# Optimization experiments

Measured on AMD Instinct MI355X. Metric: run time of the kernel, lower is better.

## Reference

```python
import jax, jax.numpy as jnp
import numpy as np

NS, NW, E, DIN, OUT, H = 100_000, 400_000, 500_000, 64, 64, 4


def setup_inputs() -> dict:
    key = jax.random.key(0)
    ks = jax.random.split(key, 26)
    s = 1.0 / np.sqrt(DIN)
    sg = 1.0 / np.sqrt(OUT)
    inp = {
        "x_sites": jax.random.normal(ks[0], (NS, DIN), jnp.float32),
        "x_wells": jax.random.normal(ks[1], (NW, DIN), jnp.float32),
        "edge_sw_src": jax.random.randint(ks[2], (E,), 0, NS, jnp.int32),
        "edge_sw_dst": jax.random.randint(ks[3], (E,), 0, NW, jnp.int32),
        "edge_ws_src": jax.random.randint(ks[4], (E,), 0, NW, jnp.int32),
        "edge_ws_dst": jax.random.randint(ks[5], (E,), 0, NS, jnp.int32),
        # GAT ('pfas_sites','distance','gw_wells'), heads=4, concat=False
        "W_sw": jax.random.normal(ks[6], (DIN, H * OUT), jnp.float32) * s,
        "att_src_sw": jax.random.normal(ks[7], (H, OUT), jnp.float32) * sg,
        "att_dst_sw": jax.random.normal(ks[8], (H, OUT), jnp.float32) * sg,
        "b_sw": jnp.zeros((OUT,), jnp.float32),
        # SAGE ('gw_wells','distance','pfas_sites')
        "Wl_ws": jax.random.normal(ks[9], (DIN, OUT), jnp.float32) * s,
        "bl_ws": jnp.zeros((OUT,), jnp.float32),
        "Wr_ws": jax.random.normal(ks[10], (DIN, OUT), jnp.float32) * s,
        # GAT ('pfas_sites','self_loop','pfas_sites'), add_self_loops=True -> identity edges
        "W_ss": jax.random.normal(ks[11], (DIN, H * OUT), jnp.float32) * s,
        "att_src_ss": jax.random.normal(ks[12], (H, OUT), jnp.float32) * sg,
        "att_dst_ss": jax.random.normal(ks[13], (H, OUT), jnp.float32) * sg,
        "b_ss": jnp.zeros((OUT,), jnp.float32),
        # SAGE ('gw_wells','self_loop','gw_wells') with identity edges
        "Wl_ww": jax.random.normal(ks[14], (DIN, OUT), jnp.float32) * s,
        "bl_ww": jnp.zeros((OUT,), jnp.float32),
        "Wr_ww": jax.random.normal(ks[15], (DIN, OUT), jnp.float32) * s,
        # output heads
        "Wg": jax.random.normal(ks[16], (OUT, 1), jnp.float32) * sg,
        "bg": jnp.zeros((1,), jnp.float32),
        "Wsit": jax.random.normal(ks[17], (OUT, 1), jnp.float32) * sg,
        "bsit": jnp.zeros((1,), jnp.float32),
    }
    return inp


def _gat(x_src, x_dst, src, dst, W, a_src, a_dst, b, n_dst):
    """PyG GATConv, concat=False (mean over heads), negative_slope=0.2."""
    h, c = a_src.shape
    xs = (x_src @ W).reshape(-1, h, c)  # [Ns,H,C]
    xd = (x_dst @ W).reshape(-1, h, c)  # [Nd,H,C]
    al_s = jnp.einsum("nhc,hc->nh", xs, a_src)
    al_d = jnp.einsum("nhc,hc->nh", xd, a_dst)
    e = jax.nn.leaky_relu(al_s[src] + al_d[dst], 0.2)  # [E,H]
    m = jax.ops.segment_max(e, dst, num_segments=n_dst)
    ex = jnp.exp(e - m[dst])
    denom = jax.ops.segment_sum(ex, dst, num_segments=n_dst)
    alpha = ex / denom[dst]  # edge-softmax per dst node
    msg = xs[src] * alpha[:, :, None]  # [E,H,C] dominant intermediate
    out = jax.ops.segment_sum(msg, dst, num_segments=n_dst)
    return out.mean(axis=1) + b


def _sage(x_src, x_dst, src, dst, Wl, bl, Wr, n_dst):
    """PyG SAGEConv, mean aggregation, root_weight=True."""
    ssum = jax.ops.segment_sum(x_src[src], dst, num_segments=n_dst)
    cnt = jax.ops.segment_sum(jnp.ones((src.shape[0],), x_src.dtype), dst, num_segments=n_dst)
    mean = ssum / jnp.maximum(cnt, 1.0)[:, None]  # empty neighborhood -> 0 (PyG mean scatter)
    return mean @ Wl + bl + x_dst @ Wr


def reference(x_sites, x_wells, edge_sw_src, edge_sw_dst, edge_ws_src, edge_ws_dst,
              W_sw, att_src_sw, att_dst_sw, b_sw, Wl_ws, bl_ws, Wr_ws,
              W_ss, att_src_ss, att_dst_ss, b_ss, Wl_ww, bl_ww, Wr_ww,
              Wg, bg, Wsit, bsit):
    # relation 1: GAT sites -> wells
    gw = _gat(x_sites, x_wells, edge_sw_src, edge_sw_dst, W_sw, att_src_sw, att_dst_sw, b_sw, NW)
    # relation 4: SAGE self-loop on wells; identity edges -> mean == x itself
    gw = gw + (x_wells @ Wl_ww + bl_ww + x_wells @ Wr_ww)  # HeteroConv aggr='sum'
    # relation 2: SAGE wells -> sites
    si = _sage(x_wells, x_sites, edge_ws_src, edge_ws_dst, Wl_ws, bl_ws, Wr_ws, NS)
    # relation 3: GAT self-loop on sites (add_self_loops=True -> identity edge set);
    # softmax over a single self edge is 1, so output = mean over heads of lin(x) + bias
    si = si + (x_sites @ W_ss).reshape(NS, H, OUT).mean(axis=1) + b_ss
    # post: relu -> dropout (eval mode: identity) -> linear -> leaky_relu(0.01)
    gw = jax.nn.relu(gw)
    si = jax.nn.relu(si)
    o_gw = jax.nn.leaky_relu(gw @ Wg + bg, 0.01)   # [NW, 1]
    o_si = jax.nn.leaky_relu(si @ Wsit + bsit, 0.01)  # [NS, 1]
    return o_gw, o_si
```

## Files before the change

### kernel.cpp

```cpp
#include <hip/hip_runtime.h>

#define NS_ 100000
#define NW_ 400000
#define NE_ 500000
#define EPB 2048

typedef float f32x4_t __attribute__((ext_vector_type(4)));
typedef unsigned u32x4_t __attribute__((ext_vector_type(4)));

__device__ __forceinline__ float lrelu02(float x) { return x > 0.f ? x : 0.2f * x; }
__device__ __forceinline__ float bf2f(unsigned short u) {
    return __uint_as_float(((unsigned)u) << 16);
}
__device__ __forceinline__ unsigned short f2bf(float f) {
    unsigned u = __float_as_uint(f);
    u += 0x7FFFu + ((u >> 16) & 1u);
    return (unsigned short)(u >> 16);
}
__device__ __forceinline__ unsigned pk(float lo, float hi) {
    return (unsigned)f2bf(lo) | ((unsigned)f2bf(hi) << 16);
}
__device__ __forceinline__ void mfma_bf16(f32x4_t& acc, u32x4_t a, u32x4_t b) {
    asm volatile("v_mfma_f32_16x16x32_bf16 %0, %1, %2, %0" : "+v"(acc) : "v"(a), "v"(b));
}

__global__ void __launch_bounds__(256)
k_prep(const float* __restrict__ W_sw, const float* __restrict__ att_src,
       const float* __restrict__ att_dst,
       const float* __restrict__ Wl_ww, const float* __restrict__ Wr_ww,
       const float* __restrict__ Wl_ws, const float* __restrict__ Wr_ws,
       const float* __restrict__ W_ss,
       float* __restrict__ vd, float* __restrict__ vs,
       u32x4_t* __restrict__ fw, u32x4_t* __restrict__ fs,
       u32x4_t* __restrict__ fsp)
{
    const int tid = threadIdx.x;
    {
        int d = tid >> 2, h = tid & 3;
        const float4* wp = (const float4*)(W_sw + d * 256 + h * 64);
        const float4* ad = (const float4*)(att_dst + h * 64);
        const float4* as = (const float4*)(att_src + h * 64);
        float accd = 0.f, accs = 0.f;
#pragma unroll
        for (int c = 0; c < 16; ++c) {
            float4 wv = wp[c]; float4 dv = ad[c]; float4 sv = as[c];
            accd += wv.x * dv.x + wv.y * dv.y + wv.z * dv.z + wv.w * dv.w;
            accs += wv.x * sv.x + wv.y * sv.y + wv.z * sv.z + wv.w * sv.w;
        }
        vd[d * 4 + h] = accd;
        vs[d * 4 + h] = accs;
    }
    for (int idx = tid; idx < 512; idx += 256) {
        int f = idx >> 6, lane = idx & 63;
        int kc = f >> 2, ct = f & 3, q = lane >> 4, n = lane & 15;
        int c = ct * 16 + n;
        u32x4_t d;
#pragma unroll
        for (int i = 0; i < 4; ++i) {
            int k = kc * 32 + q * 8 + 2 * i;
            d[i] = pk(Wl_ww[k * 64 + c] + Wr_ww[k * 64 + c],
                      Wl_ww[(k + 1) * 64 + c] + Wr_ww[(k + 1) * 64 + c]);
        }
        fw[idx] = d;
    }
    for (int idx = tid; idx < 1024; idx += 256) {
        int f = idx >> 6, lane = idx & 63;
        int kc = f >> 2, ct = f & 3, q = lane >> 4, n = lane & 15;
        int c = ct * 16 + n;
        u32x4_t d;
#pragma unroll
        for (int i = 0; i < 4; ++i) {
            int k = kc * 32 + q * 8 + 2 * i;
            float lo, hi;
            if (k < 64) {
                lo = Wl_ws[k * 64 + c];
                hi = Wl_ws[(k + 1) * 64 + c];
            } else {
                int kk = k - 64;
                lo = Wr_ws[kk * 64 + c] + 0.25f * (W_ss[kk * 256 + c] + W_ss[kk * 256 + 64 + c] +
                                                   W_ss[kk * 256 + 128 + c] + W_ss[kk * 256 + 192 + c]);
                hi = Wr_ws[(kk + 1) * 64 + c] + 0.25f * (W_ss[(kk + 1) * 256 + c] + W_ss[(kk + 1) * 256 + 64 + c] +
                                                         W_ss[(kk + 1) * 256 + 128 + c] + W_ss[(kk + 1) * 256 + 192 + c]);
            }
            d[i] = pk(lo, hi);
        }
        fs[idx] = d;
    }
    for (int idx = tid; idx < 2048; idx += 256) {
        int f = idx >> 6, lane = idx & 63;
        int kc = f >> 4, ct = f & 15, q = lane >> 4, n = lane & 15;
        int c = ct * 16 + n;
        u32x4_t d;
#pragma unroll
        for (int i = 0; i < 4; ++i) {
            int k = kc * 32 + q * 8 + 2 * i;
            d[i] = pk(W_sw[k * 256 + c], W_sw[(k + 1) * 256 + c]);
        }
        fsp[idx] = d;
    }
}

#define SP_PAD 264
__global__ void __launch_bounds__(256)
k_sites_pre(const float* __restrict__ x_sites, const u32x4_t* __restrict__ fsp,
            const float* __restrict__ vs, unsigned short* __restrict__ xs,
            float* __restrict__ al_s)
{
    __shared__ unsigned short stg[4][16 * SP_PAD];
    __shared__ float vsl[256];
    const int tid = threadIdx.x;
    vsl[tid] = vs[tid];
    __syncthreads();
    const int wave = __builtin_amdgcn_readfirstlane(tid >> 6);
    const int lane = tid & 63, q = lane >> 4, n = lane & 15;
    const int sbase = blockIdx.x * 64 + wave * 16;
    const int srow = min(sbase + n, NS_ - 1);
    const float* xr = x_sites + (size_t)srow * 64 + q * 8;
    float4 x0 = *(const float4*)(xr);
    float4 x1 = *(const float4*)(xr + 4);
    float4 x2 = *(const float4*)(xr + 32);
    float4 x3 = *(const float4*)(xr + 36);
    u32x4_t am0 = { pk(x0.x, x0.y), pk(x0.z, x0.w), pk(x1.x, x1.y), pk(x1.z, x1.w) };
    u32x4_t am1 = { pk(x2.x, x2.y), pk(x2.z, x2.w), pk(x3.x, x3.y), pk(x3.z, x3.w) };
    float pa[4];
#pragma unroll
    for (int h = 0; h < 4; ++h) {
        const float* v0 = &vsl[(q * 8) * 4 + h];
        const float* v1 = &vsl[(32 + q * 8) * 4 + h];
        pa[h] = x0.x * v0[0]  + x0.y * v0[4]  + x0.z * v0[8]  + x0.w * v0[12]
              + x1.x * v0[16] + x1.y * v0[20] + x1.z * v0[24] + x1.w * v0[28]
              + x2.x * v1[0]  + x2.y * v1[4]  + x2.z * v1[8]  + x2.w * v1[12]
              + x3.x * v1[16] + x3.y * v1[20] + x3.z * v1[24] + x3.w * v1[28];
    }
#pragma unroll
    for (int h = 0; h < 4; ++h) {
        pa[h] += __shfl_xor(pa[h], 16, 64);
        pa[h] += __shfl_xor(pa[h], 32, 64);
    }
    if (q == 0 && sbase + n < NS_)
        *(float4*)(al_s + (size_t)(sbase + n) * 4) = make_float4(pa[0], pa[1], pa[2], pa[3]);

    f32x4_t acc[16];
#pragma unroll
    for (int ct = 0; ct < 16; ++ct) acc[ct] = (f32x4_t){0, 0, 0, 0};
    asm volatile("s_nop 3" : "+v"(am0), "+v"(am1));
#pragma unroll
    for (int ct = 0; ct < 16; ++ct) mfma_bf16(acc[ct], am0, fsp[ct * 64 + lane]);
#pragma unroll
    for (int ct = 0; ct < 16; ++ct) mfma_bf16(acc[ct], am1, fsp[(16 + ct) * 64 + lane]);
    asm volatile("s_nop 7\n\ts_nop 7" ::: "memory");
    unsigned short* ss = &stg[wave][0];
#pragma unroll
    for (int ct = 0; ct < 16; ++ct)
#pragma unroll
        for (int reg = 0; reg < 4; ++reg)
            ss[(q * 4 + reg) * SP_PAD + ct * 16 + n] = f2bf(acc[ct][reg]);
    __builtin_amdgcn_s_waitcnt(0);
#pragma unroll
    for (int i = 0; i < 8; ++i) {
        int g = i * 64 + lane;
        int r = g >> 5, c = g & 31;
        if (sbase + r < NS_) {
            u32x4_t v = *(const u32x4_t*)(ss + r * SP_PAD + c * 8);
            *(u32x4_t*)(xs + (size_t)(sbase + r) * 256 + c * 8) = v;
        }
    }
}

__global__ void __launch_bounds__(256)
k_hist2(const int* __restrict__ d1, int* __restrict__ h1,
        const int* __restrict__ d2, int* __restrict__ h2)
{
    int e = blockIdx.x * 256 + threadIdx.x;
    if (e >= NE_) return;
    if (blockIdx.y == 0) atomicAdd(&h1[d1[e]], 1);
    else                 atomicAdd(&h2[d2[e]], 1);
}

__global__ void __launch_bounds__(256)
k_scan1_2(const int* __restrict__ h1, int n1, int* __restrict__ b1, int nb1,
          const int* __restrict__ h2, int n2, int* __restrict__ b2)
{
    __shared__ int red[256];
    const int tid = threadIdx.x;
    const int bx = blockIdx.x;
    const int* hist; int n; int* bsum; int blk;
    if (bx < nb1) { hist = h1; n = n1; bsum = b1; blk = bx; }
    else          { hist = h2; n = n2; bsum = b2; blk = bx - nb1; }
    int base = blk * EPB + tid * 8;
    int s = 0;
#pragma unroll
    for (int i = 0; i < 8; ++i) { int idx = base + i; if (idx < n) s += hist[idx]; }
    red[tid] = s;
    __syncthreads();
    for (int off = 128; off > 0; off >>= 1) {
        if (tid < off) red[tid] += red[tid + off];
        __syncthreads();
    }
    if (tid == 0) bsum[blk] = red[0];
}

__global__ void __launch_bounds__(256)
k_scan2_2(int* __restrict__ b1, int nb1, int* __restrict__ b2, int nb2)
{
    __shared__ int sh[256];
    const int tid = threadIdx.x;
    int* bsum = blockIdx.x == 0 ? b1 : b2;
    int nb = blockIdx.x == 0 ? nb1 : nb2;
    sh[tid] = (tid < nb) ? bsum[tid] : 0;
    __syncthreads();
    for (int off = 1; off < 256; off <<= 1) {
        int u = (tid >= off) ? sh[tid - off] : 0;
        __syncthreads();
        sh[tid] += u;
        __syncthreads();
    }
    if (tid < nb) bsum[tid] = (tid == 0) ? 0 : sh[tid - 1];
}

__global__ void __launch_bounds__(256)
k_scan3_2(const int* __restrict__ h1, int n1, const int* __restrict__ b1,
          int* __restrict__ rp1, int* __restrict__ cu1, int nb1,
          const int* __restrict__ h2, int n2, const int* __restrict__ b2,
          int* __restrict__ rp2, int* __restrict__ cu2)
{
    __shared__ int tsum[256];
    const int tid = threadIdx.x;
    const int bx = blockIdx.x;
    const int* hist; int n; const int* bsum; int* rowptr; int* cursor; int blk;
    if (bx < nb1) { hist = h1; n = n1; bsum = b1; rowptr = rp1; cursor = cu1; blk = bx; }
    else          { hist = h2; n = n2; bsum = b2; rowptr = rp2; cursor = cu2; blk = bx - nb1; }
    int base = blk * EPB + tid * 8;
    int v[8]; int s = 0;
#pragma unroll
    for (int i = 0; i < 8; ++i) {
        int idx = base + i;
        v[i] = (idx < n) ? hist[idx] : 0;
        s += v[i];
    }
    tsum[tid] = s;
    __syncthreads();
    for (int off = 1; off < 256; off <<= 1) {
        int u = (tid >= off) ? tsum[tid - off] : 0;
        __syncthreads();
        tsum[tid] += u;
        __syncthreads();
    }
    int texcl = tsum[tid] - s;
    int run = bsum[blk] + texcl;
#pragma unroll
    for (int i = 0; i < 8; ++i) {
        int idx = base + i;
        if (idx < n) { rowptr[idx] = run; cursor[idx] = run; run += v[i]; }
    }
    if (blk == 0 && tid == 0) rowptr[n] = NE_;
}

__global__ void __launch_bounds__(256)
k_scatter2(const int* __restrict__ s1, const int* __restrict__ d1,
           int* __restrict__ c1, int* __restrict__ o1,
           const int* __restrict__ s2, const int* __restrict__ d2,
           int* __restrict__ c2, int* __restrict__ o2)
{
    int e = blockIdx.x * 256 + threadIdx.x;
    if (e >= NE_) return;
    if (blockIdx.y == 0) { int p = atomicAdd(&c1[d1[e]], 1); o1[p] = s1[e]; }
    else                 { int p = atomicAdd(&c2[d2[e]], 1); o2[p] = s2[e]; }
}

__global__ void __launch_bounds__(256)
k_gat_wells(const float* __restrict__ x_wells, const float* __restrict__ vd,
            const int* __restrict__ rowptr, const int* __restrict__ csr_src,
            const float* __restrict__ al_s, const unsigned short* __restrict__ xs,
            const float* __restrict__ b_sw, const float* __restrict__ bl_ww,
            const u32x4_t* __restrict__ fw, const float* __restrict__ Wg,
            const float* __restrict__ bg, float* __restrict__ out)
{
    __shared__ float vdl[16][17];
    __shared__ float xw[16][68];
    __shared__ float dl[16][68];
    __shared__ float biasl[64];
    __shared__ float wgl[64];
    __shared__ float res[16];
    const int tid = threadIdx.x;
    vdl[tid >> 4][tid & 15] = vd[tid];
    if (tid < 64) { biasl[tid] = b_sw[tid] + bl_ww[tid]; wgl[tid] = Wg[tid]; }
    __syncthreads();
    const int wl = tid >> 4, p = tid & 15;
    const int w = blockIdx.x * 16 + wl;
    float h0, h1, h2, h3;
    {
        float4 xv = *(const float4*)(x_wells + (size_t)w * 64 + 4 * p);
        *(float4*)&xw[wl][4 * p] = xv;
        const float* vp = vdl[p];
        h0 = xv.x * vp[0] + xv.y * vp[4] + xv.z * vp[8]  + xv.w * vp[12];
        h1 = xv.x * vp[1] + xv.y * vp[5] + xv.z * vp[9]  + xv.w * vp[13];
        h2 = xv.x * vp[2] + xv.y * vp[6] + xv.z * vp[10] + xv.w * vp[14];
        h3 = xv.x * vp[3] + xv.y * vp[7] + xv.z * vp[11] + xv.w * vp[15];
    }
#pragma unroll
    for (int off = 1; off < 16; off <<= 1) {
        h0 += __shfl_xor(h0, off, 64);
        h1 += __shfl_xor(h1, off, 64);
        h2 += __shfl_xor(h2, off, 64);
        h3 += __shfl_xor(h3, off, 64);
    }
    const int r0 = rowptr[w], r1 = rowptr[w + 1];
    float den0 = 0, den1 = 0, den2 = 0, den3 = 0;
    float n0[4] = {0, 0, 0, 0}, n1[4] = {0, 0, 0, 0};
    float n2[4] = {0, 0, 0, 0}, n3[4] = {0, 0, 0, 0};
    for (int j = r0; j < r1; ++j) {
        int s = csr_src[j];
        float4 as = ((const float4*)al_s)[s];
        float e0 = __expf(lrelu02(as.x + h0));
        float e1 = __expf(lrelu02(as.y + h1));
        float e2 = __expf(lrelu02(as.z + h2));
        float e3 = __expf(lrelu02(as.w + h3));
        den0 += e0; den1 += e1; den2 += e2; den3 += e3;
        const unsigned short* xr = xs + (size_t)s * 256 + 4 * p;
        ushort4 u0 = *(const ushort4*)(xr);
        ushort4 u1 = *(const ushort4*)(xr + 64);
        ushort4 u2 = *(const ushort4*)(xr + 128);
        ushort4 u3 = *(const ushort4*)(xr + 192);
        n0[0] += e0 * bf2f(u0.x); n0[1] += e0 * bf2f(u0.y); n0[2] += e0 * bf2f(u0.z); n0[3] += e0 * bf2f(u0.w);
        n1[0] += e1 * bf2f(u1.x); n1[1] += e1 * bf2f(u1.y); n1[2] += e1 * bf2f(u1.z); n1[3] += e1 * bf2f(u1.w);
        n2[0] += e2 * bf2f(u2.x); n2[1] += e2 * bf2f(u2.y); n2[2] += e2 * bf2f(u2.z); n2[3] += e2 * bf2f(u2.w);
        n3[0] += e3 * bf2f(u3.x); n3[1] += e3 * bf2f(u3.y); n3[2] += e3 * bf2f(u3.z); n3[3] += e3 * bf2f(u3.w);
    }
    const int c0 = 4 * p;
    float tmsg[4];
    if (r1 > r0) {
        float i0 = 0.25f / den0, i1 = 0.25f / den1, i2 = 0.25f / den2, i3 = 0.25f / den3;
#pragma unroll
        for (int i = 0; i < 4; ++i)
            tmsg[i] = n0[i] * i0 + n1[i] * i1 + n2[i] * i2 + n3[i] * i3 + biasl[c0 + i];
    } else {
#pragma unroll
        for (int i = 0; i < 4; ++i) tmsg[i] = biasl[c0 + i];
    }
    __syncthreads();
    const int wave = __builtin_amdgcn_readfirstlane(tid >> 6);
    const int lane = tid & 63, q = lane >> 4, n = lane & 15;
    u32x4_t a0, a1;
#pragma unroll
    for (int i = 0; i < 4; ++i) {
        a0[i] = pk(xw[n][q * 8 + 2 * i],      xw[n][q * 8 + 2 * i + 1]);
        a1[i] = pk(xw[n][32 + q * 8 + 2 * i], xw[n][32 + q * 8 + 2 * i + 1]);
    }
    f32x4_t acc = {0, 0, 0, 0};
    asm volatile("s_nop 3" : "+v"(a0), "+v"(a1), "+v"(acc));
    mfma_bf16(acc, a0, fw[wave * 64 + lane]);
    mfma_bf16(acc, a1, fw[(4 + wave) * 64 + lane]);
    asm volatile("s_nop 7\n\ts_nop 7" : "+v"(acc));
#pragma unroll
    for (int reg = 0; reg < 4; ++reg)
        dl[q * 4 + reg][wave * 16 + n] = acc[reg];
    __syncthreads();
    float4 dv = *(const float4*)&dl[wl][c0];
    float t0 = tmsg[0] + dv.x;
    float t1 = tmsg[1] + dv.y;
    float t2 = tmsg[2] + dv.z;
    float t3 = tmsg[3] + dv.w;
    float pr = fmaxf(t0, 0.f) * wgl[c0] + fmaxf(t1, 0.f) * wgl[c0 + 1] +
               fmaxf(t2, 0.f) * wgl[c0 + 2] + fmaxf(t3, 0.f) * wgl[c0 + 3];
    pr += __shfl_xor(pr, 1, 64);
    pr += __shfl_xor(pr, 2, 64);
    pr += __shfl_xor(pr, 4, 64);
    pr += __shfl_xor(pr, 8, 64);
    if (p == 0) res[wl] = pr + bg[0];
    __syncthreads();
    if (tid < 16) {
        float v = res[tid];
        out[blockIdx.x * 16 + tid] = v > 0.f ? v : 0.01f * v;
    }
}

__global__ void __launch_bounds__(256)
k_sage_sites(const float* __restrict__ x_sites, const float* __restrict__ x_wells,
             const int* __restrict__ rowptr, const int* __restrict__ csr_src,
             const u32x4_t* __restrict__ fs, const float* __restrict__ bl_ws,
             const float* __restrict__ b_ss, const float* __restrict__ Wsit,
             const float* __restrict__ bsit, float* __restrict__ out)
{
    __shared__ float mnL[16][68];
    __shared__ float xL[16][68];
    __shared__ float dl[16][68];
    __shared__ float biasl[64];
    __shared__ float wsl[64];
    __shared__ float res[16];
    const int tid = threadIdx.x;
    if (tid < 64) { biasl[tid] = bl_ws[tid] + b_ss[tid]; wsl[tid] = Wsit[tid]; }
    const int sl = tid >> 4, p = tid & 15;
    const int s = blockIdx.x * 16 + sl;
    const int r0 = rowptr[s], r1 = rowptr[s + 1];
    float4 m4 = {0.f, 0.f, 0.f, 0.f};
    for (int j = r0; j < r1; ++j) {
        int wsrc = csr_src[j];
        float4 xv = ((const float4*)(x_wells + (size_t)wsrc * 64))[p];
        m4.x += xv.x; m4.y += xv.y; m4.z += xv.z; m4.w += xv.w;
    }
    if (r1 > r0) {
        float rc = 1.f / (float)(r1 - r0);
        m4.x *= rc; m4.y *= rc; m4.z *= rc; m4.w *= rc;
    }
    *(float4*)&mnL[sl][4 * p] = m4;
    {
        float4 xv = *(const float4*)(x_sites + (size_t)s * 64 + 4 * p);
        *(float4*)&xL[sl][4 * p] = xv;
    }
    __syncthreads();
    const int wave = __builtin_amdgcn_readfirstlane(tid >> 6);
    const int lane = tid & 63, q = lane >> 4, n = lane & 15;
    u32x4_t am0, am1, ax0, ax1;
#pragma unroll
    for (int i = 0; i < 4; ++i) {
        am0[i] = pk(mnL[n][q * 8 + 2 * i],      mnL[n][q * 8 + 2 * i + 1]);
        am1[i] = pk(mnL[n][32 + q * 8 + 2 * i], mnL[n][32 + q * 8 + 2 * i + 1]);
        ax0[i] = pk(xL[n][q * 8 + 2 * i],       xL[n][q * 8 + 2 * i + 1]);
        ax1[i] = pk(xL[n][32 + q * 8 + 2 * i],  xL[n][32 + q * 8 + 2 * i + 1]);
    }
    f32x4_t acc = {0, 0, 0, 0};
    asm volatile("s_nop 3" : "+v"(am0), "+v"(am1), "+v"(ax0), "+v"(ax1), "+v"(acc));
    mfma_bf16(acc, am0, fs[wave * 64 + lane]);
    mfma_bf16(acc, am1, fs[(4 + wave) * 64 + lane]);
    mfma_bf16(acc, ax0, fs[(8 + wave) * 64 + lane]);
    mfma_bf16(acc, ax1, fs[(12 + wave) * 64 + lane]);
    asm volatile("s_nop 7\n\ts_nop 7" : "+v"(acc));
#pragma unroll
    for (int reg = 0; reg < 4; ++reg)
        dl[q * 4 + reg][wave * 16 + n] = acc[reg];
    __syncthreads();
    const int c0 = 4 * p;
    float4 dv = *(const float4*)&dl[sl][c0];
    float t0 = dv.x + biasl[c0];
    float t1 = dv.y + biasl[c0 + 1];
    float t2 = dv.z + biasl[c0 + 2];
    float t3 = dv.w + biasl[c0 + 3];
    float pr = fmaxf(t0, 0.f) * wsl[c0] + fmaxf(t1, 0.f) * wsl[c0 + 1] +
               fmaxf(t2, 0.f) * wsl[c0 + 2] + fmaxf(t3, 0.f) * wsl[c0 + 3];
    pr += __shfl_xor(pr, 1, 64);
    pr += __shfl_xor(pr, 2, 64);
    pr += __shfl_xor(pr, 4, 64);
    pr += __shfl_xor(pr, 8, 64);
    if (p == 0) res[sl] = pr + bsit[0];
    __syncthreads();
    if (tid < 16) {
        float v = res[tid];
        out[(size_t)NW_ + blockIdx.x * 16 + tid] = v > 0.f ? v : 0.01f * v;
    }
}

extern "C" void kernel_launch(void* const* d_in, const int* in_sizes, int n_in,
                              void* d_out, int out_size, void* d_ws, size_t ws_size,
                              hipStream_t stream)
{
    const float* x_sites    = (const float*)d_in[0];
    const float* x_wells    = (const float*)d_in[1];
    const int*   e_sw_src   = (const int*)d_in[2];
    const int*   e_sw_dst   = (const int*)d_in[3];
    const int*   e_ws_src   = (const int*)d_in[4];
    const int*   e_ws_dst   = (const int*)d_in[5];
    const float* W_sw       = (const float*)d_in[6];
    const float* att_src_sw = (const float*)d_in[7];
    const float* att_dst_sw = (const float*)d_in[8];
    const float* b_sw       = (const float*)d_in[9];
    const float* Wl_ws      = (const float*)d_in[10];
    const float* bl_ws      = (const float*)d_in[11];
    const float* Wr_ws      = (const float*)d_in[12];
    const float* W_ss       = (const float*)d_in[13];
    const float* b_ss       = (const float*)d_in[16];
    const float* Wl_ww      = (const float*)d_in[17];
    const float* bl_ww      = (const float*)d_in[18];
    const float* Wr_ww      = (const float*)d_in[19];
    const float* Wg         = (const float*)d_in[20];
    const float* bg         = (const float*)d_in[21];
    const float* Wsit       = (const float*)d_in[22];
    const float* bsit       = (const float*)d_in[23];
    float* out = (float*)d_out;

    unsigned short* xs = (unsigned short*)d_ws;
    float* al_s = (float*)(xs + (size_t)NS_ * 256);
    float* vd   = al_s + (size_t)NS_ * 4;
    float* vs   = vd + 256;
    u32x4_t* fw = (u32x4_t*)(vs + 256);
    u32x4_t* fs = fw + 512;
    u32x4_t* fsp= fs + 1024;
    int* ip     = (int*)(fsp + 2048);
    int* h_sw   = ip;
    int* h_ws   = h_sw + NW_;
    int* rp_sw  = h_ws + NS_;
    int* cur_sw = rp_sw + NW_ + 4;
    int* csr_sw = cur_sw + NW_;
    int* bs_sw  = csr_sw + NE_;
    int* rp_ws  = bs_sw + 256;
    int* cur_ws = rp_ws + NS_ + 4;
    int* csr_ws = cur_ws + NS_;
    int* bs_ws  = csr_ws + NE_;

    hipMemsetAsync(h_sw, 0, (size_t)(NW_ + NS_) * sizeof(int), stream);

    const int egrid = (NE_ + 255) / 256;
    const int nb_sw = (NW_ + EPB - 1) / EPB;
    const int nb_ws = (NS_ + EPB - 1) / EPB;

    hipLaunchKernelGGL(k_hist2, dim3(egrid, 2), dim3(256), 0, stream,
                       e_sw_dst, h_sw, e_ws_dst, h_ws);
    hipLaunchKernelGGL(k_scan1_2, dim3(nb_sw + nb_ws), dim3(256), 0, stream,
                       h_sw, NW_, bs_sw, nb_sw, h_ws, NS_, bs_ws);
    hipLaunchKernelGGL(k_scan2_2, dim3(2), dim3(256), 0, stream,
                       bs_sw, nb_sw, bs_ws, nb_ws);
    hipLaunchKernelGGL(k_scan3_2, dim3(nb_sw + nb_ws), dim3(256), 0, stream,
                       h_sw, NW_, bs_sw, rp_sw, cur_sw, nb_sw,
                       h_ws, NS_, bs_ws, rp_ws, cur_ws);
    hipLaunchKernelGGL(k_scatter2, dim3(egrid, 2), dim3(256), 0, stream,
                       e_sw_src, e_sw_dst, cur_sw, csr_sw,
                       e_ws_src, e_ws_dst, cur_ws, csr_ws);

    hipLaunchKernelGGL(k_prep, dim3(1), dim3(256), 0, stream,
                       W_sw, att_src_sw, att_dst_sw, Wl_ww, Wr_ww, Wl_ws, Wr_ws, W_ss,
                       vd, vs, fw, fs, fsp);
    hipLaunchKernelGGL(k_sites_pre, dim3((NS_ + 63) / 64), dim3(256), 0, stream,
                       x_sites, fsp, vs, xs, al_s);

    hipLaunchKernelGGL(k_gat_wells, dim3(NW_ / 16), dim3(256), 0, stream,
                       x_wells, vd, rp_sw, csr_sw, al_s, xs, b_sw, bl_ww,
                       fw, Wg, bg, out);
    hipLaunchKernelGGL(k_sage_sites, dim3(NS_ / 16), dim3(256), 0, stream,
                       x_sites, x_wells, rp_ws, csr_ws, fs, bl_ws, b_ss,
                       Wsit, bsit, out);
}
```

Measured before the change: 468.5 us.

## Merge independent kernels into combined launches and pack bf16 tiles in LDS

Merges the sites precompute with the degree histogram into one launch, moves the weight prep before it, and fuses the SAGE-sites and GAT-wells aggregation kernels into one grid that branches on block index. The MFMA input tiles are now packed to bf16 when written to shared memory with a swizzled layout, instead of being converted from fp32 when read back. The goal is fewer kernel launches and inter-kernel gaps, tail overlap between independent work, and less shared-memory traffic. The cost is a larger shared-memory footprint per block in the merged kernels, which may lower occupancy for the lighter branch.

```diff
diff --git a/kernel.cpp b/kernel.cpp
--- a/kernel.cpp
+++ b/kernel.cpp
@@ -4,6 +4,11 @@
 #define NW_ 400000
 #define NE_ 500000
 #define EPB 2048
+
+#define SP_BLKS  ((NS_ + 63) / 64)
+#define HG_BLKS  ((NE_ + 255) / 256)
+#define SAGE_BLKS (NS_ / 16)
+#define GAT_BLKS  (NW_ / 16)
 
 typedef float f32x4_t __attribute__((ext_vector_type(4)));
 typedef unsigned u32x4_t __attribute__((ext_vector_type(4)));
@@ -102,18 +107,33 @@
 
 #define SP_PAD 264
 __global__ void __launch_bounds__(256)
-k_sites_pre(const float* __restrict__ x_sites, const u32x4_t* __restrict__ fsp,
-            const float* __restrict__ vs, unsigned short* __restrict__ xs,
-            float* __restrict__ al_s)
-{
-    __shared__ unsigned short stg[4][16 * SP_PAD];
-    __shared__ float vsl[256];
+k_main1(const float* __restrict__ x_sites, const u32x4_t* __restrict__ fsp,
+        const float* __restrict__ vs, unsigned short* __restrict__ xs,
+        float* __restrict__ al_s,
+        const int* __restrict__ d1, int* __restrict__ h1,
+        const int* __restrict__ d2, int* __restrict__ h2)
+{
+    __shared__ float smem1[8704];
     const int tid = threadIdx.x;
+    const int bid = blockIdx.x;
+    if (bid >= SP_BLKS) {
+        int hb = bid - SP_BLKS;
+        int rel = hb / HG_BLKS;
+        int e = (hb % HG_BLKS) * 256 + tid;
+        if (e < NE_) {
+            if (rel == 0) atomicAdd(&h1[d1[e]], 1);
+            else          atomicAdd(&h2[d2[e]], 1);
+        }
+        return;
+    }
+    unsigned short* stg = (unsigned short*)smem1;
+    float* vsl = smem1 + 8448 / 2 * 0 + 8448;
+    vsl = smem1 + 8448;
     vsl[tid] = vs[tid];
     __syncthreads();
     const int wave = __builtin_amdgcn_readfirstlane(tid >> 6);
     const int lane = tid & 63, q = lane >> 4, n = lane & 15;
-    const int sbase = blockIdx.x * 64 + wave * 16;
+    const int sbase = bid * 64 + wave * 16;
     const int srow = min(sbase + n, NS_ - 1);
     const float* xr = x_sites + (size_t)srow * 64 + q * 8;
     float4 x0 = *(const float4*)(xr);
@@ -149,7 +169,7 @@
 #pragma unroll
     for (int ct = 0; ct < 16; ++ct) mfma_bf16(acc[ct], am1, fsp[(16 + ct) * 64 + lane]);
     asm volatile("s_nop 7\n\ts_nop 7" ::: "memory");
-    unsigned short* ss = &stg[wave][0];
+    unsigned short* ss = stg + wave * (16 * SP_PAD);
 #pragma unroll
     for (int ct = 0; ct < 16; ++ct)
 #pragma unroll
@@ -165,16 +185,6 @@
             *(u32x4_t*)(xs + (size_t)(sbase + r) * 256 + c * 8) = v;
         }
     }
-}
-
-__global__ void __launch_bounds__(256)
-k_hist2(const int* __restrict__ d1, int* __restrict__ h1,
-        const int* __restrict__ d2, int* __restrict__ h2)
-{
-    int e = blockIdx.x * 256 + threadIdx.x;
-    if (e >= NE_) return;
-    if (blockIdx.y == 0) atomicAdd(&h1[d1[e]], 1);
-    else                 atomicAdd(&h2[d2[e]], 1);
 }
 
 __global__ void __launch_bounds__(256)
@@ -269,184 +279,190 @@
 }
 
 __global__ void __launch_bounds__(256)
-k_gat_wells(const float* __restrict__ x_wells, const float* __restrict__ vd,
-            const int* __restrict__ rowptr, const int* __restrict__ csr_src,
-            const float* __restrict__ al_s, const unsigned short* __restrict__ xs,
-            const float* __restrict__ b_sw, const float* __restrict__ bl_ww,
-            const u32x4_t* __restrict__ fw, const float* __restrict__ Wg,
-            const float* __restrict__ bg, float* __restrict__ out)
-{
-    __shared__ float vdl[16][17];
-    __shared__ float xw[16][68];
-    __shared__ float dl[16][68];
-    __shared__ float biasl[64];
-    __shared__ float wgl[64];
-    __shared__ float res[16];
+k_main6(const float* __restrict__ x_sites, const float* __restrict__ x_wells,
+        const int* __restrict__ rp_ws, const int* __restrict__ csr_ws,
+        const u32x4_t* __restrict__ fs, const float* __restrict__ bl_ws,
+        const float* __restrict__ b_ss, const float* __restrict__ Wsit,
+        const float* __restrict__ bsit,
+        const float* __restrict__ vd, const int* __restrict__ rp_sw,
+        const int* __restrict__ csr_sw, const float* __restrict__ al_s,
+        const unsigned short* __restrict__ xs, const float* __restrict__ b_sw,
+        const float* __restrict__ bl_ww, const u32x4_t* __restrict__ fw,
+        const float* __restrict__ Wg, const float* __restrict__ bg,
+        float* __restrict__ out)
+{
+    __shared__ float smem[2400];
     const int tid = threadIdx.x;
-    vdl[tid >> 4][tid & 15] = vd[tid];
-    if (tid < 64) { biasl[tid] = b_sw[tid] + bl_ww[tid]; wgl[tid] = Wg[tid]; }
-    __syncthreads();
-    const int wl = tid >> 4, p = tid & 15;
-    const int w = blockIdx.x * 16 + wl;
-    float h0, h1, h2, h3;
+    const int bid = blockIdx.x;
+
+    if (bid < SAGE_BLKS) {
+        unsigned* mnB = (unsigned*)smem;
+        unsigned* xB  = (unsigned*)(smem + 576);
+        float* dl     = smem + 1152;
+        float* biasl  = smem + 2240;
+        float* wsl    = smem + 2304;
+        float* res    = smem + 2368;
+        if (tid < 64) { biasl[tid] = bl_ws[tid] + b_ss[tid]; wsl[tid] = Wsit[tid]; }
+        const int sl = tid >> 4, p = tid & 15;
+        const int s = bid * 16 + sl;
+        const int r0 = rp_ws[s], r1 = rp_ws[s + 1];
+        float4 m4 = {0.f, 0.f, 0.f, 0.f};
+        for (int j = r0; j < r1; ++j) {
+            int wsrc = csr_ws[j];
+            float4 xv = ((const float4*)(x_wells + (size_t)wsrc * 64))[p];
+            m4.x += xv.x; m4.y += xv.y; m4.z += xv.z; m4.w += xv.w;
+        }
+        if (r1 > r0) {
+            float rc = 1.f / (float)(r1 - r0);
+            m4.x *= rc; m4.y *= rc; m4.z *= rc; m4.w *= rc;
+        }
+        {
+            int c0 = (2 * p + 8 * sl) & 31;
+            mnB[sl * 36 + c0]     = pk(m4.x, m4.y);
+            mnB[sl * 36 + c0 + 1] = pk(m4.z, m4.w);
+            float4 xv = *(const float4*)(x_sites + (size_t)s * 64 + 4 * p);
+            xB[sl * 36 + c0]     = pk(xv.x, xv.y);
+            xB[sl * 36 + c0 + 1] = pk(xv.z, xv.w);
+        }
+        __syncthreads();
+        const int wave = __builtin_amdgcn_readfirstlane(tid >> 6);
+        const int lane = tid & 63, q = lane >> 4, n = lane & 15;
+        const int b0 = (4 * q + 8 * n) & 31;
+        const int b1 = (16 + 4 * q + 8 * n) & 31;
+        u32x4_t am0 = *(const u32x4_t*)&mnB[n * 36 + b0];
+        u32x4_t am1 = *(const u32x4_t*)&mnB[n * 36 + b1];
+        u32x4_t ax0 = *(const u32x4_t*)&xB[n * 36 + b0];
+        u32x4_t ax1 = *(const u32x4_t*)&xB[n * 36 + b1];
+        f32x4_t acc = {0, 0, 0, 0};
+        asm volatile("s_nop 3" : "+v"(am0), "+v"(am1), "+v"(ax0), "+v"(ax1), "+v"(acc));
+        mfma_bf16(acc, am0, fs[wave * 64 + lane]);
+        mfma_bf16(acc, am1, fs[(4 + wave) * 64 + lane]);
+        mfma_bf16(acc, ax0, fs[(8 + wave) * 64 + lane]);
+        mfma_bf16(acc, ax1, fs[(12 + wave) * 64 + lane]);
+        asm volatile("s_nop 7\n\ts_nop 7" : "+v"(acc));
+#pragma unroll
+        for (int reg = 0; reg < 4; ++reg)
+            dl[(q * 4 + reg) * 68 + wave * 16 + n] = acc[reg];
+        __syncthreads();
+        const int c0 = 4 * p;
+        float4 dv = *(const float4*)&dl[sl * 68 + c0];
+        float t0 = dv.x + biasl[c0];
+        float t1 = dv.y + biasl[c0 + 1];
+        float t2 = dv.z + biasl[c0 + 2];
+        float t3 = dv.w + biasl[c0 + 3];
+        float pr = fmaxf(t0, 0.f) * wsl[c0] + fmaxf(t1, 0.f) * wsl[c0 + 1] +
+                   fmaxf(t2, 0.f) * wsl[c0 + 2] + fmaxf(t3, 0.f) * wsl[c0 + 3];
+        pr += __shfl_xor(pr, 1, 64);
+        pr += __shfl_xor(pr, 2, 64);
+        pr += __shfl_xor(pr, 4, 64);
+        pr += __shfl_xor(pr, 8, 64);
+        if (p == 0) res[sl] = pr + bsit[0];
+        __syncthreads();
+        if (tid < 16) {
+            float v = res[tid];
+            out[(size_t)NW_ + bid * 16 + tid] = v > 0.f ? v : 0.01f * v;
+        }
+        return;
+    }
+
     {
-        float4 xv = *(const float4*)(x_wells + (size_t)w * 64 + 4 * p);
-        *(float4*)&xw[wl][4 * p] = xv;
-        const float* vp = vdl[p];
-        h0 = xv.x * vp[0] + xv.y * vp[4] + xv.z * vp[8]  + xv.w * vp[12];
-        h1 = xv.x * vp[1] + xv.y * vp[5] + xv.z * vp[9]  + xv.w * vp[13];
-        h2 = xv.x * vp[2] + xv.y * vp[6] + xv.z * vp[10] + xv.w * vp[14];
-        h3 = xv.x * vp[3] + xv.y * vp[7] + xv.z * vp[11] + xv.w * vp[15];
-    }
-#pragma unroll
-    for (int off = 1; off < 16; off <<= 1) {
-        h0 += __shfl_xor(h0, off, 64);
-        h1 += __shfl_xor(h1, off, 64);
-        h2 += __shfl_xor(h2, off, 64);
-        h3 += __shfl_xor(h3, off, 64);
-    }
-    const int r0 = rowptr[w], r1 = rowptr[w + 1];
-    float den0 = 0, den1 = 0, den2 = 0, den3 = 0;
-    float n0[4] = {0, 0, 0, 0}, n1[4] = {0, 0, 0, 0};
-    float n2[4] = {0, 0, 0, 0}, n3[4] = {0, 0, 0, 0};
-    for (int j = r0; j < r1; ++j) {
-        int s = csr_src[j];
-        float4 as = ((const float4*)al_s)[s];
-        float e0 = __expf(lrelu02(as.x + h0));
-        float e1 = __expf(lrelu02(as.y + h1));
-        float e2 = __expf(lrelu02(as.z + h2));
-        float e3 = __expf(lrelu02(as.w + h3));
-        den0 += e0; den1 += e1; den2 += e2; den3 += e3;
-        const unsigned short* xr = xs + (size_t)s * 256 + 4 * p;
-        ushort4 u0 = *(const ushort4*)(xr);
-        ushort4 u1 = *(const ushort4*)(xr + 64);
-        ushort4 u2 = *(const ushort4*)(xr + 128);
-        ushort4 u3 = *(const ushort4*)(xr + 192);
-        n0[0] += e0 * bf2f(u0.x); n0[1] += e0 * bf2f(u0.y); n0[2] += e0 * bf2f(u0.z); n0[3] += e0 * bf2f(u0.w);
-        n1[0] += e1 * bf2f(u1.x); n1[1] += e1 * bf2f(u1.y); n1[2] += e1 * bf2f(u1.z); n1[3] += e1 * bf2f(u1.w);
-        n2[0] += e2 * bf2f(u2.x); n2[1] += e2 * bf2f(u2.y); n2[2] += e2 * bf2f(u2.z); n2[3] += e2 * bf2f(u2.w);
-        n3[0] += e3 * bf2f(u3.x); n3[1] += e3 * bf2f(u3.y); n3[2] += e3 * bf2f(u3.z); n3[3] += e3 * bf2f(u3.w);
-    }
-    const int c0 = 4 * p;
-    float tmsg[4];
-    if (r1 > r0) {
-        float i0 = 0.25f / den0, i1 = 0.25f / den1, i2 = 0.25f / den2, i3 = 0.25f / den3;
-#pragma unroll
-        for (int i = 0; i < 4; ++i)
-            tmsg[i] = n0[i] * i0 + n1[i] * i1 + n2[i] * i2 + n3[i] * i3 + biasl[c0 + i];
-    } else {
-#pragma unroll
-        for (int i = 0; i < 4; ++i) tmsg[i] = biasl[c0 + i];
-    }
-    __syncthreads();
-    const int wave = __builtin_amdgcn_readfirstlane(tid >> 6);
-    const int lane = tid & 63, q = lane >> 4, n = lane & 15;
-    u32x4_t a0, a1;
-#pragma unroll
-    for (int i = 0; i < 4; ++i) {
-        a0[i] = pk(xw[n][q * 8 + 2 * i],      xw[n][q * 8 + 2 * i + 1]);
-        a1[i] = pk(xw[n][32 + q * 8 + 2 * i], xw[n][32 + q * 8 + 2 * i + 1]);
-    }
-    f32x4_t acc = {0, 0, 0, 0};
-    asm volatile("s_nop 3" : "+v"(a0), "+v"(a1), "+v"(acc));
-    mfma_bf16(acc, a0, fw[wave * 64 + lane]);
-    mfma_bf16(acc, a1, fw[(4 + wave) * 64 + lane]);
-    asm volatile("s_nop 7\n\ts_nop 7" : "+v"(acc));
-#pragma unroll
-    for (int reg = 0; reg < 4; ++reg)
-        dl[q * 4 + reg][wave * 16 + n] = acc[reg];
-    __syncthreads();
-    float4 dv = *(const float4*)&dl[wl][c0];
-    float t0 = tmsg[0] + dv.x;
-    float t1 = tmsg[1] + dv.y;
-    float t2 = tmsg[2] + dv.z;
-    float t3 = tmsg[3] + dv.w;
-    float pr = fmaxf(t0, 0.f) * wgl[c0] + fmaxf(t1, 0.f) * wgl[c0 + 1] +
-               fmaxf(t2, 0.f) * wgl[c0 + 2] + fmaxf(t3, 0.f) * wgl[c0 + 3];
-    pr += __shfl_xor(pr, 1, 64);
-    pr += __shfl_xor(pr, 2, 64);
-    pr += __shfl_xor(pr, 4, 64);
-    pr += __shfl_xor(pr, 8, 64);
-    if (p == 0) res[wl] = pr + bg[0];
-    __syncthreads();
-    if (tid < 16) {
-        float v = res[tid];
-        out[blockIdx.x * 16 + tid] = v > 0.f ? v : 0.01f * v;
-    }
-}
-
-__global__ void __launch_bounds__(256)
-k_sage_sites(const float* __restrict__ x_sites, const float* __restrict__ x_wells,
-             const int* __restrict__ rowptr, const int* __restrict__ csr_src,
-             const u32x4_t* __restrict__ fs, const float* __restrict__ bl_ws,
-             const float* __restrict__ b_ss, const float* __restrict__ Wsit,
-             const float* __restrict__ bsit, float* __restrict__ out)
-{
-    __shared__ float mnL[16][68];
-    __shared__ float xL[16][68];
-    __shared__ float dl[16][68];
-    __shared__ float biasl[64];
-    __shared__ float wsl[64];
-    __shared__ float res[16];
-    const int tid = threadIdx.x;
-    if (tid < 64) { biasl[tid] = bl_ws[tid] + b_ss[tid]; wsl[tid] = Wsit[tid]; }
-    const int sl = tid >> 4, p = tid & 15;
-    const int s = blockIdx.x * 16 + sl;
-    const int r0 = rowptr[s], r1 = rowptr[s + 1];
-    float4 m4 = {0.f, 0.f, 0.f, 0.f};
-    for (int j = r0; j < r1; ++j) {
-        int wsrc = csr_src[j];
-        float4 xv = ((const float4*)(x_wells + (size_t)wsrc * 64))[p];
-        m4.x += xv.x; m4.y += xv.y; m4.z += xv.z; m4.w += xv.w;
-    }
-    if (r1 > r0) {
-        float rc = 1.f / (float)(r1 - r0);
-        m4.x *= rc; m4.y *= rc; m4.z *= rc; m4.w *= rc;
-    }
-    *(float4*)&mnL[sl][4 * p] = m4;
-    {
-        float4 xv = *(const float4*)(x_sites + (size_t)s * 64 + 4 * p);
-        *(float4*)&xL[sl][4 * p] = xv;
-    }
-    __syncthreads();
-    const int wave = __builtin_amdgcn_readfirstlane(tid >> 6);
-    const int lane = tid & 63, q = lane >> 4, n = lane & 15;
-    u32x4_t am0, am1, ax0, ax1;
-#pragma unroll
-    for (int i = 0; i < 4; ++i) {
-        am0[i] = pk(mnL[n][q * 8 + 2 * i],      mnL[n][q * 8 + 2 * i + 1]);
-        am1[i] = pk(mnL[n][32 + q * 8 + 2 * i], mnL[n][32 + q * 8 + 2 * i + 1]);
-        ax0[i] = pk(xL[n][q * 8 + 2 * i],       xL[n][q * 8 + 2 * i + 1]);
-        ax1[i] = pk(xL[n][32 + q * 8 + 2 * i],  xL[n][32 + q * 8 + 2 * i + 1]);
-    }
-    f32x4_t acc = {0, 0, 0, 0};
-    asm volatile("s_nop 3" : "+v"(am0), "+v"(am1), "+v"(ax0), "+v"(ax1), "+v"(acc));
-    mfma_bf16(acc, am0, fs[wave * 64 + lane]);
-    mfma_bf16(acc, am1, fs[(4 + wave) * 64 + lane]);
-    mfma_bf16(acc, ax0, fs[(8 + wave) * 64 + lane]);
-    mfma_bf16(acc, ax1, fs[(12 + wave) * 64 + lane]);
-    asm volatile("s_nop 7\n\ts_nop 7" : "+v"(acc));
-#pragma unroll
-    for (int reg = 0; reg < 4; ++reg)
-        dl[q * 4 + reg][wave * 16 + n] = acc[reg];
-    __syncthreads();
-    const int c0 = 4 * p;
-    float4 dv = *(const float4*)&dl[sl][c0];
-    float t0 = dv.x + biasl[c0];
-    float t1 = dv.y + biasl[c0 + 1];
-    float t2 = dv.z + biasl[c0 + 2];
-    float t3 = dv.w + biasl[c0 + 3];
-    float pr = fmaxf(t0, 0.f) * wsl[c0] + fmaxf(t1, 0.f) * wsl[c0 + 1] +
-               fmaxf(t2, 0.f) * wsl[c0 + 2] + fmaxf(t3, 0.f) * wsl[c0 + 3];
-    pr += __shfl_xor(pr, 1, 64);
-    pr += __shfl_xor(pr, 2, 64);
-    pr += __shfl_xor(pr, 4, 64);
-    pr += __shfl_xor(pr, 8, 64);
-    if (p == 0) res[sl] = pr + bsit[0];
-    __syncthreads();
-    if (tid < 16) {
-        float v = res[tid];
-        out[(size_t)NW_ + blockIdx.x * 16 + tid] = v > 0.f ? v : 0.01f * v;
+        const int gb = bid - SAGE_BLKS;
+        float* vdl    = smem;
+        unsigned* xwB = (unsigned*)(smem + 272);
+        float* dl     = smem + 848;
+        float* biasl  = smem + 1936;
+        float* wgl    = smem + 2000;
+        float* res    = smem + 2064;
+        vdl[(tid >> 4) * 17 + (tid & 15)] = vd[tid];
+        if (tid < 64) { biasl[tid] = b_sw[tid] + bl_ww[tid]; wgl[tid] = Wg[tid]; }
+        __syncthreads();
+        const int wl = tid >> 4, p = tid & 15;
+        const int w = gb * 16 + wl;
+        const int r0 = rp_sw[w], r1 = rp_sw[w + 1];
+        float h0, h1, h2, h3;
+        {
+            float4 xv = *(const float4*)(x_wells + (size_t)w * 64 + 4 * p);
+            int c0 = (2 * p + 8 * wl) & 31;
+            xwB[wl * 36 + c0]     = pk(xv.x, xv.y);
+            xwB[wl * 36 + c0 + 1] = pk(xv.z, xv.w);
+            const float* vp = &vdl[p * 17];
+            h0 = xv.x * vp[0] + xv.y * vp[4] + xv.z * vp[8]  + xv.w * vp[12];
+            h1 = xv.x * vp[1] + xv.y * vp[5] + xv.z * vp[9]  + xv.w * vp[13];
+            h2 = xv.x * vp[2] + xv.y * vp[6] + xv.z * vp[10] + xv.w * vp[14];
+            h3 = xv.x * vp[3] + xv.y * vp[7] + xv.z * vp[11] + xv.w * vp[15];
+        }
+#pragma unroll
+        for (int off = 1; off < 16; off <<= 1) {
+            h0 += __shfl_xor(h0, off, 64);
+            h1 += __shfl_xor(h1, off, 64);
+            h2 += __shfl_xor(h2, off, 64);
+            h3 += __shfl_xor(h3, off, 64);
+        }
+        float den0 = 0, den1 = 0, den2 = 0, den3 = 0;
+        float n0[4] = {0, 0, 0, 0}, n1[4] = {0, 0, 0, 0};
+        float n2[4] = {0, 0, 0, 0}, n3[4] = {0, 0, 0, 0};
+        for (int j = r0; j < r1; ++j) {
+            int s = csr_sw[j];
+            float4 as = ((const float4*)al_s)[s];
+            float e0 = __expf(lrelu02(as.x + h0));
+            float e1 = __expf(lrelu02(as.y + h1));
+            float e2 = __expf(lrelu02(as.z + h2));
+            float e3 = __expf(lrelu02(as.w + h3));
+            den0 += e0; den1 += e1; den2 += e2; den3 += e3;
+            const unsigned short* xr = xs + (size_t)s * 256 + 4 * p;
+            ushort4 u0 = *(const ushort4*)(xr);
+            ushort4 u1 = *(const ushort4*)(xr + 64);
+            ushort4 u2 = *(const ushort4*)(xr + 128);
+            ushort4 u3 = *(const ushort4*)(xr + 192);
+            n0[0] += e0 * bf2f(u0.x); n0[1] += e0 * bf2f(u0.y); n0[2] += e0 * bf2f(u0.z); n0[3] += e0 * bf2f(u0.w);
+            n1[0] += e1 * bf2f(u1.x); n1[1] += e1 * bf2f(u1.y); n1[2] += e1 * bf2f(u1.z); n1[3] += e1 * bf2f(u1.w);
+            n2[0] += e2 * bf2f(u2.x); n2[1] += e2 * bf2f(u2.y); n2[2] += e2 * bf2f(u2.z); n2[3] += e2 * bf2f(u2.w);
+            n3[0] += e3 * bf2f(u3.x); n3[1] += e3 * bf2f(u3.y); n3[2] += e3 * bf2f(u3.z); n3[3] += e3 * bf2f(u3.w);
+        }
+        const int c0 = 4 * p;
+        float tmsg[4];
+        if (r1 > r0) {
+            float i0 = 0.25f / den0, i1 = 0.25f / den1, i2 = 0.25f / den2, i3 = 0.25f / den3;
+#pragma unroll
+            for (int i = 0; i < 4; ++i)
+                tmsg[i] = n0[i] * i0 + n1[i] * i1 + n2[i] * i2 + n3[i] * i3 + biasl[c0 + i];
+        } else {
+#pragma unroll
+            for (int i = 0; i < 4; ++i) tmsg[i] = biasl[c0 + i];
+        }
+        __syncthreads();
+        const int wave = __builtin_amdgcn_readfirstlane(tid >> 6);
+        const int lane = tid & 63, q = lane >> 4, n = lane & 15;
+        const int b0 = (4 * q + 8 * n) & 31;
+        const int b1 = (16 + 4 * q + 8 * n) & 31;
+        u32x4_t ax0 = *(const u32x4_t*)&xwB[n * 36 + b0];
+        u32x4_t ax1 = *(const u32x4_t*)&xwB[n * 36 + b1];
+        f32x4_t acc = {0, 0, 0, 0};
+        asm volatile("s_nop 3" : "+v"(ax0), "+v"(ax1), "+v"(acc));
+        mfma_bf16(acc, ax0, fw[wave * 64 + lane]);
+        mfma_bf16(acc, ax1, fw[(4 + wave) * 64 + lane]);
+        asm volatile("s_nop 7\n\ts_nop 7" : "+v"(acc));
+#pragma unroll
+        for (int reg = 0; reg < 4; ++reg)
+            dl[(q * 4 + reg) * 68 + wave * 16 + n] = acc[reg];
+        __syncthreads();
+        float4 dv = *(const float4*)&dl[wl * 68 + c0];
+        float t0 = tmsg[0] + dv.x;
+        float t1 = tmsg[1] + dv.y;
+        float t2 = tmsg[2] + dv.z;
+        float t3 = tmsg[3] + dv.w;
+        float pr = fmaxf(t0, 0.f) * wgl[c0] + fmaxf(t1, 0.f) * wgl[c0 + 1] +
+                   fmaxf(t2, 0.f) * wgl[c0 + 2] + fmaxf(t3, 0.f) * wgl[c0 + 3];
+        pr += __shfl_xor(pr, 1, 64);
+        pr += __shfl_xor(pr, 2, 64);
+        pr += __shfl_xor(pr, 4, 64);
+        pr += __shfl_xor(pr, 8, 64);
+        if (p == 0) res[wl] = pr + bg[0];
+        __syncthreads();
+        if (tid < 16) {
+            float v = res[tid];
+            out[gb * 16 + tid] = v > 0.f ? v : 0.01f * v;
+        }
     }
 }
 
@@ -499,12 +515,18 @@
 
     hipMemsetAsync(h_sw, 0, (size_t)(NW_ + NS_) * sizeof(int), stream);
 
-    const int egrid = (NE_ + 255) / 256;
+    const int egrid = HG_BLKS;
     const int nb_sw = (NW_ + EPB - 1) / EPB;
     const int nb_ws = (NS_ + EPB - 1) / EPB;
 
-    hipLaunchKernelGGL(k_hist2, dim3(egrid, 2), dim3(256), 0, stream,
+    hipLaunchKernelGGL(k_prep, dim3(1), dim3(256), 0, stream,
+                       W_sw, att_src_sw, att_dst_sw, Wl_ww, Wr_ww, Wl_ws, Wr_ws, W_ss,
+                       vd, vs, fw, fs, fsp);
+
+    hipLaunchKernelGGL(k_main1, dim3(SP_BLKS + 2 * HG_BLKS), dim3(256), 0, stream,
+                       x_sites, fsp, vs, xs, al_s,
                        e_sw_dst, h_sw, e_ws_dst, h_ws);
+
     hipLaunchKernelGGL(k_scan1_2, dim3(nb_sw + nb_ws), dim3(256), 0, stream,
                        h_sw, NW_, bs_sw, nb_sw, h_ws, NS_, bs_ws);
     hipLaunchKernelGGL(k_scan2_2, dim3(2), dim3(256), 0, stream,
@@ -516,16 +538,7 @@
                        e_sw_src, e_sw_dst, cur_sw, csr_sw,
                        e_ws_src, e_ws_dst, cur_ws, csr_ws);
 
-    hipLaunchKernelGGL(k_prep, dim3(1), dim3(256), 0, stream,
-                       W_sw, att_src_sw, att_dst_sw, Wl_ww, Wr_ww, Wl_ws, Wr_ws, W_ss,
-                       vd, vs, fw, fs, fsp);
-    hipLaunchKernelGGL(k_sites_pre, dim3((NS_ + 63) / 64), dim3(256), 0, stream,
-                       x_sites, fsp, vs, xs, al_s);
-
-    hipLaunchKernelGGL(k_gat_wells, dim3(NW_ / 16), dim3(256), 0, stream,
-                       x_wells, vd, rp_sw, csr_sw, al_s, xs, b_sw, bl_ww,
-                       fw, Wg, bg, out);
-    hipLaunchKernelGGL(k_sage_sites, dim3(NS_ / 16), dim3(256), 0, stream,
-                       x_sites, x_wells, rp_ws, csr_ws, fs, bl_ws, b_ss,
-                       Wsit, bsit, out);
-}
+    hipLaunchKernelGGL(k_main6, dim3(SAGE_BLKS + GAT_BLKS), dim3(256), 0, stream,
+                       x_sites, x_wells, rp_ws, csr_ws, fs, bl_ws, b_ss, Wsit, bsit,
+                       vd, rp_sw, csr_sw, al_s, xs, b_sw, bl_ww, fw, Wg, bg, out);
+}
```

Result: slower. 481.8 us (+2.8%).
